# Kernel optimization log

Measured on AMD Instinct MI355X. Metric: run time of the kernel, lower is better.

The kernel has to match this reference:

```python
import math
import jax, jax.numpy as jnp
import numpy as np

NUM_HEADS = 8
HEAD_DIM = 64
SCALE = 1.0 / math.sqrt(HEAD_DIM)


def setup_inputs() -> dict:
    key = jax.random.key(0)
    k1, k2, k3, k4 = jax.random.split(key, 4)
    B, C, H, W = 8, 256, 32, 32
    hidden = NUM_HEADS * HEAD_DIM  # 512
    x = jax.random.normal(k1, (B, C, H, W), dtype=jnp.float32)
    Wqkv = jax.random.normal(k2, (3 * hidden, C), dtype=jnp.float32) * 0.02  # 1x1 conv, no bias
    Wout = jax.random.normal(k3, (C, hidden), dtype=jnp.float32) * 0.02      # 1x1 conv weight
    bout = jax.random.normal(k4, (C,), dtype=jnp.float32) * 0.02             # 1x1 conv bias
    return {"x": x, "Wqkv": Wqkv, "Wout": Wout, "bout": bout}


def reference(x, Wqkv, Wout, bout):
    B, C, H, W = x.shape
    n = H * W
    # _AttLayer: 1x1 conv -> channels ordered (k=3, heads, head_dim)
    qkv = jnp.einsum('bcxy,oc->boxy', x, Wqkv)            # [B, 3*h*d, H, W]
    qkv = qkv.reshape(B, 3, NUM_HEADS, HEAD_DIM, n)       # 'b (k h d) x y -> b k h d (x y)'
    Q, K, V = qkv[:, 0], qkv[:, 1], qkv[:, 2]             # each [B, h, d, n]
    # CalcAtt: scaled QK^T, stable softmax over j, then Att @ V
    att = jnp.einsum('bhdi,bhdj->bhij', Q, K) * SCALE     # [B, h, n, n]
    att = jax.nn.softmax(att, axis=-1)                    # softmax already subtracts amax
    out = jnp.einsum('bhij,bhdj->bhid', att, V)           # [B, h, n, d]
    # 'b h (x y) d -> b (h d) x y'
    out = out.transpose(0, 1, 3, 2).reshape(B, NUM_HEADS * HEAD_DIM, H, W)
    # _AttOutLayer: 1x1 conv with bias
    return jnp.einsum('boxy,co->bcxy', out, Wout) + bout[None, :, None, None]
```

## Files before the change

kernel.cpp:

```cpp
#include <hip/hip_runtime.h>
#include <math.h>

#define NH 8
#define HD 64
#define NTOK 1024
#define CIN 256
#define HIDDEN 512
#define O3 1536
#define BATCH 8
#define ATT_SCALE 0.125f

typedef unsigned short u16;
typedef __attribute__((ext_vector_type(8))) short s16x8;
typedef __attribute__((ext_vector_type(4))) float f32x4;
typedef __attribute__((ext_vector_type(4))) unsigned short u16x4;

__device__ __forceinline__ u16 f2bf(float f) {
    union { float f; unsigned int u; } v; v.f = f;
    v.u += 0x7fff + ((v.u >> 16) & 1);
    return (u16)(v.u >> 16);
}
__device__ __forceinline__ float bf2f(u16 h) {
    union { unsigned int u; float f; } v; v.u = (unsigned)h << 16;
    return v.f;
}
__device__ __forceinline__ void split2(float x, u16& hi, u16& lo) {
    const u16 h = f2bf(x);
    hi = h;
    lo = f2bf(x - bf2f(h));
}

__device__ __forceinline__ s16x8 ldf(const u16* buf, int row, int chunk) {
    const int byte = (row * 128 + chunk * 16) ^ ((row & 7) << 4);
    return *(const s16x8*)((const char*)buf + byte);
}
__device__ __forceinline__ void st32(u16* buf, int row, int ch, s16x8 a, s16x8 b) {
    char* p = (char*)buf;
    *(s16x8*)(p + ((row * 128 + ch * 32) ^ ((row & 7) << 4)))      = a;
    *(s16x8*)(p + ((row * 128 + ch * 32 + 16) ^ ((row & 7) << 4))) = b;
}
__device__ __forceinline__ void st_stage(u16* buf, int t, s16x8 v0, s16x8 v1) {
    const int row = t >> 2, ch = t & 3;
    *(s16x8*)((char*)buf + ((row * 128 + ch * 16)       ^ ((row & 7) << 4))) = v0;
    *(s16x8*)((char*)buf + ((row * 128 + (ch + 4) * 16) ^ ((row & 7) << 4))) = v1;
}
__device__ __forceinline__ float hmax4(f32x4 v) {
    return fmaxf(fmaxf(v[0], v[1]), fmaxf(v[2], v[3]));
}
__device__ __forceinline__ float hsum4(f32x4 v) {
    return (v[0] + v[1]) + (v[2] + v[3]);
}

__global__ __launch_bounds__(256)
void split_f32(const float* __restrict__ src, u16* __restrict__ hi,
               u16* __restrict__ lo, int n4)
{
    const int i = blockIdx.x * 256 + threadIdx.x;
    if (i >= n4) return;
    const float4 v = ((const float4*)src)[i];
    u16 h0,h1,h2,h3,l0,l1,l2,l3;
    split2(v.x,h0,l0); split2(v.y,h1,l1); split2(v.z,h2,l2); split2(v.w,h3,l3);
    u16x4 H = {h0,h1,h2,h3}, L = {l0,l1,l2,l3};
    ((u16x4*)hi)[i] = H;
    ((u16x4*)lo)[i] = L;
}

__global__ __launch_bounds__(256)
void xpose_x(const float* __restrict__ x, u16* __restrict__ xthi,
             u16* __restrict__ xtlo)
{
    __shared__ float T[64][68];
    const int t  = threadIdx.x;
    const int p0 = blockIdx.x * 64;
    const int c0 = blockIdx.y * 64;
    const int b  = blockIdx.z;
    const int cl = t >> 4, pj = (t & 15) * 4;
    #pragma unroll
    for (int k = 0; k < 4; ++k)
        *(float4*)&T[cl + 16 * k][pj] =
            *(const float4*)&x[((size_t)b * CIN + c0 + cl + 16 * k) * NTOK + p0 + pj];
    __syncthreads();
    const int p = t >> 2, ch = t & 3;
    u16* dhi = xthi + ((size_t)b * NTOK + p0 + p) * CIN + c0 + ch * 16;
    u16* dlo = xtlo + ((size_t)b * NTOK + p0 + p) * CIN + c0 + ch * 16;
    #pragma unroll
    for (int g = 0; g < 2; ++g) {
        s16x8 H, L;
        #pragma unroll
        for (int e = 0; e < 8; ++e) {
            u16 hh, ll;
            split2(T[ch * 16 + g * 8 + e][p], hh, ll);
            H[e] = (short)hh; L[e] = (short)ll;
        }
        *(s16x8*)(dhi + g * 8) = H;
        *(s16x8*)(dlo + g * 8) = L;
    }
}

__global__ __launch_bounds__(256, 4)
void gemm_qkv_mfma(const u16* __restrict__ Whi, const u16* __restrict__ Wlo,
                   const u16* __restrict__ Xhi, const u16* __restrict__ Xlo,
                   u16* __restrict__ qkt, u16* __restrict__ vd)
{
    __shared__ __align__(16) char smem[32768];
    u16* Ah = (u16*)smem;
    u16* Al = (u16*)(smem + 8192);
    u16* Bh = (u16*)(smem + 16384);
    u16* Bl = (u16*)(smem + 24576);

    const int t = threadIdx.x;
    const int lane = t & 63, w = t >> 6;
    const int lr = lane & 15, lq = lane >> 4;
    const int p0 = blockIdx.x * 64;
    const int m0 = blockIdx.y * 64;
    const int b  = blockIdx.z;
    const int row = t >> 2, ch = t & 3;

    const u16* wh = Whi + (size_t)(m0 + row) * CIN + ch * 16;
    const u16* wl = Wlo + (size_t)(m0 + row) * CIN + ch * 16;
    const u16* xh = Xhi + ((size_t)b * NTOK + p0 + row) * CIN + ch * 16;
    const u16* xl = Xlo + ((size_t)b * NTOK + p0 + row) * CIN + ch * 16;

    f32x4 acc[4] = {};
    for (int kc = 0; kc < CIN; kc += 64) {
        __syncthreads();
        st32(Ah, row, ch, *(const s16x8*)(wh + kc), *(const s16x8*)(wh + kc + 8));
        st32(Al, row, ch, *(const s16x8*)(wl + kc), *(const s16x8*)(wl + kc + 8));
        st32(Bh, row, ch, *(const s16x8*)(xh + kc), *(const s16x8*)(xh + kc + 8));
        st32(Bl, row, ch, *(const s16x8*)(xl + kc), *(const s16x8*)(xl + kc + 8));
        __syncthreads();
        #pragma unroll
        for (int ks = 0; ks < 2; ++ks) {
            const s16x8 ah = ldf(Ah, w * 16 + lr, ks * 4 + lq);
            const s16x8 al = ldf(Al, w * 16 + lr, ks * 4 + lq);
            #pragma unroll
            for (int js = 0; js < 4; ++js) {
                const s16x8 bh = ldf(Bh, js * 16 + lr, ks * 4 + lq);
                const s16x8 bl = ldf(Bl, js * 16 + lr, ks * 4 + lq);
                acc[js] = __builtin_amdgcn_mfma_f32_16x16x32_bf16(ah, bh, acc[js], 0, 0, 0);
                acc[js] = __builtin_amdgcn_mfma_f32_16x16x32_bf16(al, bh, acc[js], 0, 0, 0);
                acc[js] = __builtin_amdgcn_mfma_f32_16x16x32_bf16(ah, bl, acc[js], 0, 0, 0);
            }
        }
    }

    __syncthreads();
    u16* T = Ah;
    char* Tc = (char*)T;
    if (m0 < 1024) {
        const float scale = (m0 < 512) ? ATT_SCALE : 1.0f;
        #pragma unroll
        for (int js = 0; js < 4; ++js) {
            const int p = js * 16 + lr;
            #pragma unroll
            for (int r = 0; r < 4; ++r) {
                const int o = w * 16 + lq * 4 + r;
                *(u16*)(Tc + ((p * 128 + o * 2) ^ ((p & 7) << 4))) = f2bf(acc[js][r] * scale);
            }
        }
        __syncthreads();
        const int sidx = (m0 < 512) ? 0 : 1;
        const int h = (m0 & 511) >> 6;
        u16* dst = qkt + ((((size_t)b * 2 + sidx) * NH + h) * NTOK + p0 + row) * 64 + ch * 16;
        *(s16x8*)dst       = *(const s16x8*)(Tc + ((row * 128 + ch * 32)      ^ ((row & 7) << 4)));
        *(s16x8*)(dst + 8) = *(const s16x8*)(Tc + ((row * 128 + ch * 32 + 16) ^ ((row & 7) << 4)));
    } else {
        const int h = (m0 - 1024) >> 6;
        #pragma unroll
        for (int js = 0; js < 4; ++js) {
            const int p = js * 16 + lr;
            #pragma unroll
            for (int r = 0; r < 4; ++r) {
                const int o = w * 16 + lq * 4 + r;
                *(u16*)(Tc + ((o * 128 + p * 2) ^ ((o & 7) << 4))) = f2bf(acc[js][r]);
            }
        }
        __syncthreads();
        u16* dst = vd + (((size_t)b * NH + h) * 64 + row) * NTOK + p0 + ch * 16;
        *(s16x8*)dst       = *(const s16x8*)(Tc + ((row * 128 + ch * 32)      ^ ((row & 7) << 4)));
        *(s16x8*)(dst + 8) = *(const s16x8*)(Tc + ((row * 128 + ch * 32 + 16) ^ ((row & 7) << 4)));
    }
}

__global__ __launch_bounds__(256, 4)
void attn_kernel(const u16* __restrict__ qkt, const u16* __restrict__ vd,
                 float* __restrict__ attn_out)
{
    __shared__ __align__(16) u16 Qt[64 * 64];
    __shared__ __align__(16) u16 Kt[64 * 64];
    __shared__ __align__(16) u16 Vt[64 * 64];
    __shared__ __align__(16) u16 Ps[64 * 64];

    const int t    = threadIdx.x;
    const int lane = t & 63;
    const int w    = t >> 6;
    const int lr   = lane & 15;
    const int lq   = lane >> 4;

    const int bid     = blockIdx.x;
    const int logical = (bid & 7) * 128 + (bid >> 3);
    const int it = logical & 15;
    const int h  = (logical >> 4) & 7;
    const int b  = logical >> 7;
    const int i0 = it * 64;

    const int srow = t >> 2, sch = t & 3;
    const u16* qg = qkt + ((((size_t)b * 2 + 0) * NH + h) * NTOK + i0 + srow) * 64 + sch * 8;
    const u16* kg = qkt + ((((size_t)b * 2 + 1) * NH + h) * NTOK + srow) * 64 + sch * 8;
    const u16* vg = vd  + (((size_t)b * NH + h) * 64 + srow) * NTOK + sch * 8;

    st_stage(Qt, t, *(const s16x8*)qg, *(const s16x8*)(qg + 32));

    s16x8 k0 = *(const s16x8*)kg, k1 = *(const s16x8*)(kg + 32);
    s16x8 v0 = *(const s16x8*)vg, v1 = *(const s16x8*)(vg + 32);

    f32x4 o0 = {0.f,0.f,0.f,0.f}, o1 = o0, o2 = o0, o3 = o0;
    float m_run = -INFINITY, l_run = 0.0f;

    const int ii = w * 16 + lr;
    char* pr = (char*)Ps;

    for (int jt = 0; jt < 16; ++jt) {
        __syncthreads();
        st_stage(Kt, t, k0, k1);
        st_stage(Vt, t, v0, v1);
        const int jn = (jt + 1) & 15;
        k0 = *(const s16x8*)(kg + (size_t)jn * 4096);
        k1 = *(const s16x8*)(kg + (size_t)jn * 4096 + 32);
        v0 = *(const s16x8*)(vg + (size_t)jn * 64);
        v1 = *(const s16x8*)(vg + (size_t)jn * 64 + 32);
        __syncthreads();

        f32x4 s0 = {0.f,0.f,0.f,0.f}, s1 = s0, s2 = s0, s3 = s0;
        #pragma unroll
        for (int ks = 0; ks < 2; ++ks) {
            const s16x8 qb = ldf(Qt, w * 16 + lr, ks * 4 + lq);
            s0 = __builtin_amdgcn_mfma_f32_16x16x32_bf16(ldf(Kt,      lr, ks*4+lq), qb, s0, 0,0,0);
            s1 = __builtin_amdgcn_mfma_f32_16x16x32_bf16(ldf(Kt, 16 + lr, ks*4+lq), qb, s1, 0,0,0);
            s2 = __builtin_amdgcn_mfma_f32_16x16x32_bf16(ldf(Kt, 32 + lr, ks*4+lq), qb, s2, 0,0,0);
            s3 = __builtin_amdgcn_mfma_f32_16x16x32_bf16(ldf(Kt, 48 + lr, ks*4+lq), qb, s3, 0,0,0);
        }

        float mt = fmaxf(fmaxf(hmax4(s0), hmax4(s1)), fmaxf(hmax4(s2), hmax4(s3)));
        mt = fmaxf(mt, __shfl_xor(mt, 16));
        mt = fmaxf(mt, __shfl_xor(mt, 32));
        const float mnew = fmaxf(m_run, mt);
        const float corr = __expf(m_run - mnew);
        f32x4 p0v, p1v, p2v, p3v;
        #pragma unroll
        for (int r = 0; r < 4; ++r) {
            p0v[r] = __expf(s0[r] - mnew);
            p1v[r] = __expf(s1[r] - mnew);
            p2v[r] = __expf(s2[r] - mnew);
            p3v[r] = __expf(s3[r] - mnew);
        }
        float lt = (hsum4(p0v) + hsum4(p1v)) + (hsum4(p2v) + hsum4(p3v));
        lt += __shfl_xor(lt, 16);
        lt += __shfl_xor(lt, 32);
        l_run = l_run * corr + lt;
        m_run = mnew;

        {
            u16x4 a = { f2bf(p0v[0]), f2bf(p0v[1]), f2bf(p0v[2]), f2bf(p0v[3]) };
            u16x4 bq= { f2bf(p1v[0]), f2bf(p1v[1]), f2bf(p1v[2]), f2bf(p1v[3]) };
            u16x4 c = { f2bf(p2v[0]), f2bf(p2v[1]), f2bf(p2v[2]), f2bf(p2v[3]) };
            u16x4 d = { f2bf(p3v[0]), f2bf(p3v[1]), f2bf(p3v[2]), f2bf(p3v[3]) };
            *(u16x4*)(pr + ((ii * 128 + ( 0 + lq * 4) * 2) ^ ((ii & 7) << 4))) = a;
            *(u16x4*)(pr + ((ii * 128 + (16 + lq * 4) * 2) ^ ((ii & 7) << 4))) = bq;
            *(u16x4*)(pr + ((ii * 128 + (32 + lq * 4) * 2) ^ ((ii & 7) << 4))) = c;
            *(u16x4*)(pr + ((ii * 128 + (48 + lq * 4) * 2) ^ ((ii & 7) << 4))) = d;
        }

        o0 *= corr; o1 *= corr; o2 *= corr; o3 *= corr;

        #pragma unroll
        for (int ks = 0; ks < 2; ++ks) {
            const s16x8 pb = ldf(Ps, w * 16 + lr, ks * 4 + lq);
            o0 = __builtin_amdgcn_mfma_f32_16x16x32_bf16(ldf(Vt,      lr, ks*4+lq), pb, o0, 0,0,0);
            o1 = __builtin_amdgcn_mfma_f32_16x16x32_bf16(ldf(Vt, 16 + lr, ks*4+lq), pb, o1, 0,0,0);
            o2 = __builtin_amdgcn_mfma_f32_16x16x32_bf16(ldf(Vt, 32 + lr, ks*4+lq), pb, o2, 0,0,0);
            o3 = __builtin_amdgcn_mfma_f32_16x16x32_bf16(ldf(Vt, 48 + lr, ks*4+lq), pb, o3, 0,0,0);
        }
    }

    const float inv = 1.0f / l_run;
    float* og = attn_out + (((size_t)b * NH + h) * 64) * NTOK + i0 + w * 16 + lr;
    #pragma unroll
    for (int r = 0; r < 4; ++r) {
        og[(size_t)( 0 + lq * 4 + r) * NTOK] = o0[r] * inv;
        og[(size_t)(16 + lq * 4 + r) * NTOK] = o1[r] * inv;
        og[(size_t)(32 + lq * 4 + r) * NTOK] = o2[r] * inv;
        og[(size_t)(48 + lq * 4 + r) * NTOK] = o3[r] * inv;
    }
}

__global__ __launch_bounds__(256, 4)
void gemm_out_mfma(const u16* __restrict__ Whi, const u16* __restrict__ Wlo,
                   const float* __restrict__ attn, const float* __restrict__ bias,
                   float* __restrict__ out)
{
    __shared__ __align__(16) char smem[24576];
    u16* Ah = (u16*)smem;
    u16* Al = (u16*)(smem + 8192);
    u16* Bt = (u16*)(smem + 16384);

    const int t = threadIdx.x;
    const int lane = t & 63, w = t >> 6;
    const int lr = lane & 15, lq = lane >> 4;
    const int p0 = blockIdx.x * 64;
    const int m0 = blockIdx.y * 64;
    const int b  = blockIdx.z;
    const int row = t >> 2, ch = t & 3;

    const u16* wh = Whi + (size_t)(m0 + row) * HIDDEN + ch * 16;
    const u16* wl = Wlo + (size_t)(m0 + row) * HIDDEN + ch * 16;
    const float* ab = attn + (size_t)b * HIDDEN * NTOK + p0;
    const int btok = t & 63;
    const int bog  = (t >> 6) * 16;

    f32x4 acc[4] = {};
    for (int kc = 0; kc < HIDDEN; kc += 64) {
        __syncthreads();
        st32(Ah, row, ch, *(const s16x8*)(wh + kc), *(const s16x8*)(wh + kc + 8));
        st32(Al, row, ch, *(const s16x8*)(wl + kc), *(const s16x8*)(wl + kc + 8));
        {
            s16x8 H0, H1;
            #pragma unroll
            for (int e = 0; e < 8; ++e)
                H0[e] = (short)f2bf(ab[(size_t)(kc + bog + e) * NTOK + btok]);
            #pragma unroll
            for (int e = 0; e < 8; ++e)
                H1[e] = (short)f2bf(ab[(size_t)(kc + bog + 8 + e) * NTOK + btok]);
            char* bp = (char*)Bt;
            *(s16x8*)(bp + ((btok * 128 + bog * 2)      ^ ((btok & 7) << 4))) = H0;
            *(s16x8*)(bp + ((btok * 128 + bog * 2 + 16) ^ ((btok & 7) << 4))) = H1;
        }
        __syncthreads();
        #pragma unroll
        for (int ks = 0; ks < 2; ++ks) {
            const s16x8 ah = ldf(Ah, w * 16 + lr, ks * 4 + lq);
            const s16x8 al = ldf(Al, w * 16 + lr, ks * 4 + lq);
            #pragma unroll
            for (int js = 0; js < 4; ++js) {
                const s16x8 bh = ldf(Bt, js * 16 + lr, ks * 4 + lq);
                acc[js] = __builtin_amdgcn_mfma_f32_16x16x32_bf16(ah, bh, acc[js], 0, 0, 0);
                acc[js] = __builtin_amdgcn_mfma_f32_16x16x32_bf16(al, bh, acc[js], 0, 0, 0);
            }
        }
    }

    __syncthreads();
    float* T = (float*)smem;
    #pragma unroll
    for (int js = 0; js < 4; ++js) {
        const int p = js * 16 + lr;
        #pragma unroll
        for (int r = 0; r < 4; ++r)
            T[(w * 16 + lq * 4 + r) * 68 + p] = acc[js][r];
    }
    __syncthreads();
    const float bv = bias[m0 + row];
    float* dst = out + ((size_t)b * CIN + m0 + row) * NTOK + p0;
    #pragma unroll
    for (int q = 0; q < 4; ++q) {
        float4 v = *(const float4*)&T[row * 68 + ch * 4 + q * 16];
        v.x += bv; v.y += bv; v.z += bv; v.w += bv;
        *(float4*)&dst[ch * 4 + q * 16] = v;
    }
}

extern "C" void kernel_launch(void* const* d_in, const int* in_sizes, int n_in,
                              void* d_out, int out_size, void* d_ws, size_t ws_size,
                              hipStream_t stream)
{
    const float* x    = (const float*)d_in[0];
    const float* Wqkv = (const float*)d_in[1];
    const float* Wout = (const float*)d_in[2];
    const float* bout = (const float*)d_in[3];
    float* out = (float*)d_out;

    char* ws = (char*)d_ws;
    u16* Wqhi = (u16*)ws;                         ws += (size_t)O3 * CIN * 2;
    u16* Wqlo = (u16*)ws;                         ws += (size_t)O3 * CIN * 2;
    u16* Wohi = (u16*)ws;                         ws += (size_t)CIN * HIDDEN * 2;
    u16* Wolo = (u16*)ws;                         ws += (size_t)CIN * HIDDEN * 2;
    u16* xThi = (u16*)ws;                         ws += (size_t)BATCH * NTOK * CIN * 2;
    u16* xTlo = (u16*)ws;                         ws += (size_t)BATCH * NTOK * CIN * 2;
    u16* qkt  = (u16*)ws;                         ws += (size_t)BATCH * 2 * NH * NTOK * HD * 2;
    u16* vd   = (u16*)ws;                         ws += (size_t)BATCH * NH * HD * NTOK * 2;
    float* attn = (float*)ws;                     ws += (size_t)BATCH * HIDDEN * NTOK * 4;

    split_f32<<<dim3(O3 * CIN / 1024), 256, 0, stream>>>(Wqkv, Wqhi, Wqlo, O3 * CIN / 4);
    split_f32<<<dim3(CIN * HIDDEN / 1024), 256, 0, stream>>>(Wout, Wohi, Wolo, CIN * HIDDEN / 4);
    xpose_x<<<dim3(16, 4, BATCH), 256, 0, stream>>>(x, xThi, xTlo);

    gemm_qkv_mfma<<<dim3(16, 24, BATCH), 256, 0, stream>>>(Wqhi, Wqlo, xThi, xTlo, qkt, vd);
    attn_kernel<<<dim3(1024), 256, 0, stream>>>(qkt, vd, attn);
    gemm_out_mfma<<<dim3(16, 4, BATCH), 256, 0, stream>>>(Wohi, Wolo, attn, bout, out);
}
```

Measured before the change: 144.6 us.

## Double-buffer K/V tiles, use exp2 softmax, merge weight-split launches

The attention kernel now stages two K/V tiles per barrier pair into separate shared buffers and prefetches the next two, halving the number of block synchronisations. Softmax switches from exp to exp2, with log2(e) folded into the Q scale inside the QKV GEMM epilogue. The two weight-splitting kernels are merged into one launch to save launch overhead. The extra shared memory and registers lower the occupancy hint from 4 to 3 blocks per CU.

```diff
diff --git a/kernel.cpp b/kernel.cpp
--- a/kernel.cpp
+++ b/kernel.cpp
@@ -9,6 +9,7 @@
 #define O3 1536
 #define BATCH 8
 #define ATT_SCALE 0.125f
+#define LOG2E 1.44269504f
 
 typedef unsigned short u16;
 typedef __attribute__((ext_vector_type(8))) short s16x8;
@@ -52,11 +53,19 @@
 }
 
 __global__ __launch_bounds__(256)
-void split_f32(const float* __restrict__ src, u16* __restrict__ hi,
-               u16* __restrict__ lo, int n4)
-{
-    const int i = blockIdx.x * 256 + threadIdx.x;
-    if (i >= n4) return;
+void split_both(const float* __restrict__ srcA, u16* __restrict__ hiA,
+                u16* __restrict__ loA, int n4A,
+                const float* __restrict__ srcB, u16* __restrict__ hiB,
+                u16* __restrict__ loB, int n4B)
+{
+    int i = blockIdx.x * 256 + threadIdx.x;
+    const float* src; u16 *hi, *lo;
+    if (i < n4A) { src = srcA; hi = hiA; lo = loA; }
+    else {
+        i -= n4A;
+        if (i >= n4B) return;
+        src = srcB; hi = hiB; lo = loB;
+    }
     const float4 v = ((const float4*)src)[i];
     u16 h0,h1,h2,h3,l0,l1,l2,l3;
     split2(v.x,h0,l0); split2(v.y,h1,l1); split2(v.z,h2,l2); split2(v.w,h3,l3);
@@ -148,7 +157,7 @@
     u16* T = Ah;
     char* Tc = (char*)T;
     if (m0 < 1024) {
-        const float scale = (m0 < 512) ? ATT_SCALE : 1.0f;
+        const float scale = (m0 < 512) ? ATT_SCALE * LOG2E : 1.0f;
         #pragma unroll
         for (int js = 0; js < 4; ++js) {
             const int p = js * 16 + lr;
@@ -182,13 +191,15 @@
     }
 }
 
-__global__ __launch_bounds__(256, 4)
+__global__ __launch_bounds__(256, 3)
 void attn_kernel(const u16* __restrict__ qkt, const u16* __restrict__ vd,
                  float* __restrict__ attn_out)
 {
     __shared__ __align__(16) u16 Qt[64 * 64];
-    __shared__ __align__(16) u16 Kt[64 * 64];
-    __shared__ __align__(16) u16 Vt[64 * 64];
+    __shared__ __align__(16) u16 Kt0[64 * 64];
+    __shared__ __align__(16) u16 Vt0[64 * 64];
+    __shared__ __align__(16) u16 Kt1[64 * 64];
+    __shared__ __align__(16) u16 Vt1[64 * 64];
     __shared__ __align__(16) u16 Ps[64 * 64];
 
     const int t    = threadIdx.x;
@@ -211,8 +222,10 @@
 
     st_stage(Qt, t, *(const s16x8*)qg, *(const s16x8*)(qg + 32));
 
-    s16x8 k0 = *(const s16x8*)kg, k1 = *(const s16x8*)(kg + 32);
-    s16x8 v0 = *(const s16x8*)vg, v1 = *(const s16x8*)(vg + 32);
+    s16x8 ka0 = *(const s16x8*)kg,          ka1 = *(const s16x8*)(kg + 32);
+    s16x8 kb0 = *(const s16x8*)(kg + 4096), kb1 = *(const s16x8*)(kg + 4096 + 32);
+    s16x8 va0 = *(const s16x8*)vg,          va1 = *(const s16x8*)(vg + 32);
+    s16x8 vb0 = *(const s16x8*)(vg + 64),   vb1 = *(const s16x8*)(vg + 64 + 32);
 
     f32x4 o0 = {0.f,0.f,0.f,0.f}, o1 = o0, o2 = o0, o3 = o0;
     float m_run = -INFINITY, l_run = 0.0f;
@@ -220,17 +233,7 @@
     const int ii = w * 16 + lr;
     char* pr = (char*)Ps;
 
-    for (int jt = 0; jt < 16; ++jt) {
-        __syncthreads();
-        st_stage(Kt, t, k0, k1);
-        st_stage(Vt, t, v0, v1);
-        const int jn = (jt + 1) & 15;
-        k0 = *(const s16x8*)(kg + (size_t)jn * 4096);
-        k1 = *(const s16x8*)(kg + (size_t)jn * 4096 + 32);
-        v0 = *(const s16x8*)(vg + (size_t)jn * 64);
-        v1 = *(const s16x8*)(vg + (size_t)jn * 64 + 32);
-        __syncthreads();
-
+    auto process_tile = [&](const u16* Kt, const u16* Vt) {
         f32x4 s0 = {0.f,0.f,0.f,0.f}, s1 = s0, s2 = s0, s3 = s0;
         #pragma unroll
         for (int ks = 0; ks < 2; ++ks) {
@@ -245,14 +248,14 @@
         mt = fmaxf(mt, __shfl_xor(mt, 16));
         mt = fmaxf(mt, __shfl_xor(mt, 32));
         const float mnew = fmaxf(m_run, mt);
-        const float corr = __expf(m_run - mnew);
+        const float corr = exp2f(m_run - mnew);
         f32x4 p0v, p1v, p2v, p3v;
         #pragma unroll
         for (int r = 0; r < 4; ++r) {
-            p0v[r] = __expf(s0[r] - mnew);
-            p1v[r] = __expf(s1[r] - mnew);
-            p2v[r] = __expf(s2[r] - mnew);
-            p3v[r] = __expf(s3[r] - mnew);
+            p0v[r] = exp2f(s0[r] - mnew);
+            p1v[r] = exp2f(s1[r] - mnew);
+            p2v[r] = exp2f(s2[r] - mnew);
+            p3v[r] = exp2f(s3[r] - mnew);
         }
         float lt = (hsum4(p0v) + hsum4(p1v)) + (hsum4(p2v) + hsum4(p3v));
         lt += __shfl_xor(lt, 16);
@@ -281,6 +284,28 @@
             o2 = __builtin_amdgcn_mfma_f32_16x16x32_bf16(ldf(Vt, 32 + lr, ks*4+lq), pb, o2, 0,0,0);
             o3 = __builtin_amdgcn_mfma_f32_16x16x32_bf16(ldf(Vt, 48 + lr, ks*4+lq), pb, o3, 0,0,0);
         }
+    };
+
+    for (int itr = 0; itr < 8; ++itr) {
+        __syncthreads();
+        st_stage(Kt0, t, ka0, ka1);
+        st_stage(Vt0, t, va0, va1);
+        st_stage(Kt1, t, kb0, kb1);
+        st_stage(Vt1, t, vb0, vb1);
+        const int jA = (2 * itr + 2) & 15;
+        const int jB = (2 * itr + 3) & 15;
+        ka0 = *(const s16x8*)(kg + (size_t)jA * 4096);
+        ka1 = *(const s16x8*)(kg + (size_t)jA * 4096 + 32);
+        kb0 = *(const s16x8*)(kg + (size_t)jB * 4096);
+        kb1 = *(const s16x8*)(kg + (size_t)jB * 4096 + 32);
+        va0 = *(const s16x8*)(vg + (size_t)jA * 64);
+        va1 = *(const s16x8*)(vg + (size_t)jA * 64 + 32);
+        vb0 = *(const s16x8*)(vg + (size_t)jB * 64);
+        vb1 = *(const s16x8*)(vg + (size_t)jB * 64 + 32);
+        __syncthreads();
+
+        process_tile(Kt0, Vt0);
+        process_tile(Kt1, Vt1);
     }
 
     const float inv = 1.0f / l_run;
@@ -390,8 +415,9 @@
     u16* vd   = (u16*)ws;                         ws += (size_t)BATCH * NH * HD * NTOK * 2;
     float* attn = (float*)ws;                     ws += (size_t)BATCH * HIDDEN * NTOK * 4;
 
-    split_f32<<<dim3(O3 * CIN / 1024), 256, 0, stream>>>(Wqkv, Wqhi, Wqlo, O3 * CIN / 4);
-    split_f32<<<dim3(CIN * HIDDEN / 1024), 256, 0, stream>>>(Wout, Wohi, Wolo, CIN * HIDDEN / 4);
+    const int n4A = O3 * CIN / 4, n4B = CIN * HIDDEN / 4;
+    split_both<<<dim3((n4A + n4B + 255) / 256), 256, 0, stream>>>(
+        Wqkv, Wqhi, Wqlo, n4A, Wout, Wohi, Wolo, n4B);
     xpose_x<<<dim3(16, 4, BATCH), 256, 0, stream>>>(x, xThi, xTlo);
 
     gemm_qkv_mfma<<<dim3(16, 24, BATCH), 256, 0, stream>>>(Wqhi, Wqlo, xThi, xTlo, qkt, vd);
```

Measured after the change: 155.6 us. 1.08x slower.
